# Kernel optimization log

Measured on AMD Instinct MI355X. Metric: run time of the kernel, lower is better.

The kernel has to match this reference:

```python
import jax, jax.numpy as jnp
import numpy as np

HEADS = 8
DIM_HEAD = 64
BOTTLENECK = 40


def setup_inputs() -> dict:
    key = jax.random.key(0)
    ks = jax.random.split(key, 10)
    b, n, qs = 4, 1024, 256
    inner = HEADS * DIM_HEAD
    s = lambda fan_in: 1.0 / np.sqrt(fan_in)
    return {
        "x":   jax.random.normal(ks[0], (b, n, qs), dtype=jnp.float32),
        # weights stored as (in, out) so forward is x @ W
        "wq1": jax.random.normal(ks[1], (qs, BOTTLENECK), dtype=jnp.float32) * s(qs),
        "wq2": jax.random.normal(ks[2], (BOTTLENECK, inner), dtype=jnp.float32) * s(BOTTLENECK),
        "wk1": jax.random.normal(ks[3], (qs, BOTTLENECK), dtype=jnp.float32) * s(qs),
        "wk2": jax.random.normal(ks[4], (BOTTLENECK, inner), dtype=jnp.float32) * s(BOTTLENECK),
        "wv1": jax.random.normal(ks[5], (qs, BOTTLENECK), dtype=jnp.float32) * s(qs),
        "wv2": jax.random.normal(ks[6], (BOTTLENECK, inner), dtype=jnp.float32) * s(BOTTLENECK),
        "wo":  jax.random.normal(ks[7], (inner, qs), dtype=jnp.float32) * s(inner),
        "bo":  jax.random.normal(ks[8], (qs,), dtype=jnp.float32) * 0.01,
    }


def reference(x, wq1, wq2, wk1, wk2, wv1, wv2, wo, bo):
    b, n, _ = x.shape
    h, d = HEADS, DIM_HEAD
    scale = d ** -0.5

    # bottlenecked QKV projections (40-dim), SiLU on K bottleneck
    q = (x @ wq1) @ wq2                       # (b, n, h*d)
    k = jax.nn.silu(x @ wk1) @ wk2            # (b, n, h*d)
    v = (x @ wv1) @ wv2                       # (b, n, h*d)

    def split(t):  # 'b n (h d) -> b (h n) d'
        return t.reshape(b, n, h, d).transpose(0, 2, 1, 3).reshape(b, h * n, d)

    q, k, v = split(q), split(k), split(v)

    sim = jnp.einsum('bid,bjd->bij', q, k) * scale   # (b, h*n, h*n)
    attn = jax.nn.softmax(sim, axis=-1)
    out = jnp.einsum('bij,bjd->bid', attn, v)        # (b, h*n, d)

    # 'b (h n) d -> b n (h d)'
    out = out.reshape(b, h, n, d).transpose(0, 2, 1, 3).reshape(b, n, h * d)
    return out @ wo + bo
```

## Files before the change

kernel.cpp:

```cpp
#include <hip/hip_runtime.h>
#include <hip/hip_bf16.h>


#define B_    4
#define H_    8
#define NSEQ  1024
#define SEQ   8192
#define DH    64
#define QS    256
#define INNER 512
#define QSCALE 0.18033688011112042f

#define KVSW_BATCH 524288

typedef __bf16 bf16x8 __attribute__((ext_vector_type(8)));
typedef float floatx4 __attribute__((ext_vector_type(4)));

__global__ __launch_bounds__(512, 4) void qkv_kernel(
    const float* __restrict__ x,
    const float* __restrict__ wq1, const float* __restrict__ wq2,
    const float* __restrict__ wk1, const float* __restrict__ wk2,
    const float* __restrict__ wv1, const float* __restrict__ wv2,
    __hip_bfloat16* __restrict__ Qg, __hip_bfloat16* __restrict__ KSg,
    __hip_bfloat16* __restrict__ VSg)
{
  const int tid  = threadIdx.x;
  const int p    = blockIdx.x >> 8;
  const int rest = blockIdx.x & 255;
  const int b    = rest >> 6;
  const int nblk = rest & 63;
  const int n0   = nblk << 4;

  __shared__ __align__(16) float xs[16][260];
  __shared__ __align__(16) float tb2[4][16][40];
  __shared__ __align__(16) float tb[16][40];
  __shared__ __align__(16) __hip_bfloat16 ob[10400];

  const float* w1 = (p == 0) ? wq1 : (p == 1) ? wk1 : wv1;
  const float* w2 = (p == 0) ? wq2 : (p == 1) ? wk2 : wv2;

  #pragma unroll
  for (int j = 0; j < 2; ++j) {
    const int i  = tid + j * 512;
    const int r  = i >> 6;
    const int c4 = (i & 63) << 2;
    *(float4*)(&xs[r][c4]) =
        *(const float4*)(x + ((size_t)b * NSEQ + n0 + r) * QS + c4);
  }
  __syncthreads();

  for (int t = tid; t < 640; t += 512) {
    const int ks  = t / 160;
    const int rem = t - ks * 160;
    const int r   = rem / 10;
    const int bn  = (rem - r * 10) * 4;
    float a0 = 0.f, a1 = 0.f, a2 = 0.f, a3 = 0.f;
    #pragma unroll 4
    for (int c4 = ks * 16; c4 < ks * 16 + 16; ++c4) {
      const float4 xv = *(const float4*)(&xs[r][c4 * 4]);
      const float4 wa = *(const float4*)(w1 + (c4 * 4 + 0) * 40 + bn);
      const float4 wb = *(const float4*)(w1 + (c4 * 4 + 1) * 40 + bn);
      const float4 wc = *(const float4*)(w1 + (c4 * 4 + 2) * 40 + bn);
      const float4 wd = *(const float4*)(w1 + (c4 * 4 + 3) * 40 + bn);
      a0 += xv.x * wa.x + xv.y * wb.x + xv.z * wc.x + xv.w * wd.x;
      a1 += xv.x * wa.y + xv.y * wb.y + xv.z * wc.y + xv.w * wd.y;
      a2 += xv.x * wa.z + xv.y * wb.z + xv.z * wc.z + xv.w * wd.z;
      a3 += xv.x * wa.w + xv.y * wb.w + xv.z * wc.w + xv.w * wd.w;
    }
    tb2[ks][r][bn + 0] = a0; tb2[ks][r][bn + 1] = a1;
    tb2[ks][r][bn + 2] = a2; tb2[ks][r][bn + 3] = a3;
  }
  __syncthreads();

  if (tid < 160) {
    const int r  = tid / 10;
    const int bn = (tid - r * 10) * 4;
    const float4 h0 = *(const float4*)(&tb2[0][r][bn]);
    const float4 h1 = *(const float4*)(&tb2[1][r][bn]);
    const float4 h2 = *(const float4*)(&tb2[2][r][bn]);
    const float4 h3 = *(const float4*)(&tb2[3][r][bn]);
    float a0 = (h0.x + h1.x) + (h2.x + h3.x);
    float a1 = (h0.y + h1.y) + (h2.y + h3.y);
    float a2 = (h0.z + h1.z) + (h2.z + h3.z);
    float a3 = (h0.w + h1.w) + (h2.w + h3.w);
    if (p == 1) {
      a0 = a0 / (1.f + __expf(-a0));
      a1 = a1 / (1.f + __expf(-a1));
      a2 = a2 / (1.f + __expf(-a2));
      a3 = a3 / (1.f + __expf(-a3));
    }
    tb[r][bn + 0] = a0; tb[r][bn + 1] = a1;
    tb[r][bn + 2] = a2; tb[r][bn + 3] = a3;
  }
  __syncthreads();

  {
    const int cq = tid & 127;
    const int rq = tid >> 7;
    const int c  = cq * 4, r0 = rq * 4;
    const float scale = (p == 0) ? QSCALE : 1.0f;
    float acc[4][4];
    #pragma unroll
    for (int i = 0; i < 4; ++i)
      #pragma unroll
      for (int j = 0; j < 4; ++j) acc[i][j] = 0.f;

    #pragma unroll 2
    for (int jb = 0; jb < 10; ++jb) {
      const float4 w0  = *(const float4*)(w2 + (jb * 4 + 0) * INNER + c);
      const float4 w1r = *(const float4*)(w2 + (jb * 4 + 1) * INNER + c);
      const float4 w2r = *(const float4*)(w2 + (jb * 4 + 2) * INNER + c);
      const float4 w3  = *(const float4*)(w2 + (jb * 4 + 3) * INNER + c);
      #pragma unroll
      for (int ri = 0; ri < 4; ++ri) {
        const float4 tv = *(const float4*)(&tb[r0 + ri][jb * 4]);
        acc[ri][0] += tv.x * w0.x + tv.y * w1r.x + tv.z * w2r.x + tv.w * w3.x;
        acc[ri][1] += tv.x * w0.y + tv.y * w1r.y + tv.z * w2r.y + tv.w * w3.y;
        acc[ri][2] += tv.x * w0.z + tv.y * w1r.z + tv.z * w2r.z + tv.w * w3.z;
        acc[ri][3] += tv.x * w0.w + tv.y * w1r.w + tv.z * w2r.w + tv.w * w3.w;
      }
    }
    #pragma unroll
    for (int ri = 0; ri < 4; ++ri)
      #pragma unroll
      for (int ci = 0; ci < 4; ++ci) {
        const int cc = c + ci;
        const float v = acc[ri][ci] * scale;
        if (p == 2) ob[cc * 20 + r0 + ri]    = __float2bfloat16(v);
        else        ob[(r0 + ri) * 520 + cc] = __float2bfloat16(v);
      }
  }
  __syncthreads();

  if (p == 0) {
    #pragma unroll
    for (int j = 0; j < 2; ++j) {
      const int i  = tid + j * 512;
      const int h  = i >> 7;
      const int r  = (i >> 3) & 15;
      const int d8 = i & 7;
      *(float4*)(Qg + ((size_t)b * SEQ + h * NSEQ + n0 + r) * DH + d8 * 8) =
          *(const float4*)(&ob[r * 520 + h * 64 + d8 * 8]);
    }
  } else if (p == 1) {
    #pragma unroll
    for (int j = 0; j < 2; ++j) {
      const int i    = tid + j * 512;
      const int h    = i >> 7;
      const int ks2  = (i >> 6) & 1;
      const int quad = (i >> 4) & 3;
      const int r    = i & 15;
      const int lane = quad * 16 + r;
      const size_t dst = (size_t)b * KVSW_BATCH
          + ((size_t)((h * 64 + nblk) * 2 + ks2) * 64 + lane) * 8;
      *(float4*)(KSg + dst) = *(const float4*)(&ob[r * 520 + h * 64 + ks2 * 32 + quad * 8]);
    }
  } else {
    const int st  = nblk & 1;
    const int p32 = nblk >> 1;
    #pragma unroll
    for (int pass = 0; pass < 4; ++pass) {
      const int i   = tid + pass * 512;
      const int h   = i >> 8;
      const int dnt = (i >> 6) & 3;
      const int dm  = (i >> 2) & 15;
      const int rg  = i & 3;
      const int lane = rg * 16 + dm;
      const size_t dst = (size_t)b * KVSW_BATCH
          + ((size_t)((h * 32 + p32) * 4 + dnt) * 64 + lane) * 8 + st * 4;
      *(uint2*)(VSg + dst) = *(const uint2*)(&ob[(h * 64 + dnt * 16 + dm) * 20 + rg * 4]);
    }
  }
}

struct PairBuf {
  bf16x8 k[2][2];
  bf16x8 v[4];
};

__global__ __launch_bounds__(256, 3) void attn_kernel(
    const __hip_bfloat16* __restrict__ Qg,
    const __hip_bfloat16* __restrict__ KSg,
    const __hip_bfloat16* __restrict__ VSg,
    float* __restrict__ OPg,
    float* __restrict__ PSg)
{
  __shared__ float Osh[4][16][68];
  __shared__ float psums[4][64];

  const int tid  = threadIdx.x;
  const int wave = tid >> 6;
  const int lane = tid & 63;
  const int lrow = lane & 15;
  const int quad = lane >> 4;

  const int xcd   = blockIdx.x & 7;
  const int idx   = blockIdx.x >> 3;
  const int b     = xcd >> 1;
  const int half  = idx & 1;
  const int qtile = (xcd & 1) * 64 + (idx >> 1);
  const int qbase = qtile * 64;

  const __hip_bfloat16* Qb  = Qg + ((size_t)b * SEQ + qbase) * DH;
  const __hip_bfloat16* kp0 = KSg + (size_t)b * KVSW_BATCH + half * 262144
                              + (size_t)wave * 65536 + lane * 8;
  const __hip_bfloat16* vp0 = VSg + (size_t)b * KVSW_BATCH + half * 262144
                              + (size_t)wave * 65536 + lane * 8;

  bf16x8 qf[4][2];
  #pragma unroll
  for (int mt = 0; mt < 4; ++mt)
    #pragma unroll
    for (int s = 0; s < 2; ++s)
      qf[mt][s] = *(const bf16x8*)(Qb + (mt * 16 + lrow) * DH + s * 32 + quad * 8);

  floatx4 oacc[4][4];
  #pragma unroll
  for (int mt = 0; mt < 4; ++mt)
    #pragma unroll
    for (int dnt = 0; dnt < 4; ++dnt)
      oacc[mt][dnt] = (floatx4){0.f, 0.f, 0.f, 0.f};
  float psum[4] = {0.f, 0.f, 0.f, 0.f};

  #pragma unroll 2
  for (int pair = 0; pair < 32; ++pair) {
    PairBuf pb;
    const __hip_bfloat16* kp = kp0 + pair * 2048;
    pb.k[0][0] = *(const bf16x8*)(kp);
    pb.k[0][1] = *(const bf16x8*)(kp + 512);
    pb.k[1][0] = *(const bf16x8*)(kp + 1024);
    pb.k[1][1] = *(const bf16x8*)(kp + 1536);
    const __hip_bfloat16* vp = vp0 + pair * 2048;
    #pragma unroll
    for (int dnt = 0; dnt < 4; ++dnt)
      pb.v[dnt] = *(const bf16x8*)(vp + dnt * 512);

    #pragma unroll
    for (int mt = 0; mt < 4; ++mt) {
      floatx4 s0 = (floatx4){0.f, 0.f, 0.f, 0.f};
      floatx4 s1 = (floatx4){0.f, 0.f, 0.f, 0.f};
      s0 = __builtin_amdgcn_mfma_f32_16x16x32_bf16(pb.k[0][0], qf[mt][0], s0, 0, 0, 0);
      s0 = __builtin_amdgcn_mfma_f32_16x16x32_bf16(pb.k[0][1], qf[mt][1], s0, 0, 0, 0);
      s1 = __builtin_amdgcn_mfma_f32_16x16x32_bf16(pb.k[1][0], qf[mt][0], s1, 0, 0, 0);
      s1 = __builtin_amdgcn_mfma_f32_16x16x32_bf16(pb.k[1][1], qf[mt][1], s1, 0, 0, 0);
      float p[8];
      #pragma unroll
      for (int r = 0; r < 4; ++r) {
        p[r]     = __builtin_amdgcn_exp2f(s0[r]);
        p[4 + r] = __builtin_amdgcn_exp2f(s1[r]);
      }
      psum[mt] += ((p[0] + p[1]) + (p[2] + p[3])) + ((p[4] + p[5]) + (p[6] + p[7]));
      bf16x8 pa;
      #pragma unroll
      for (int j = 0; j < 8; ++j) pa[j] = (__bf16)p[j];
      #pragma unroll
      for (int dnt = 0; dnt < 4; ++dnt)
        oacc[mt][dnt] = __builtin_amdgcn_mfma_f32_16x16x32_bf16(pa, pb.v[dnt], oacc[mt][dnt], 0, 0, 0);
    }
  }

  #pragma unroll
  for (int mt = 0; mt < 4; ++mt) {
    float s = psum[mt];
    s += __shfl_xor(s, 16, 64);
    s += __shfl_xor(s, 32, 64);
    psum[mt] = s;
  }
  if (quad == 0) {
    #pragma unroll
    for (int mt = 0; mt < 4; ++mt)
      psums[wave][mt * 16 + lrow] = psum[mt];
  }

  const size_t opbase = ((size_t)half * B_ + b) * SEQ + qbase;

  #pragma unroll
  for (int mt = 0; mt < 4; ++mt) {
    #pragma unroll
    for (int dnt = 0; dnt < 4; ++dnt)
      #pragma unroll
      for (int r = 0; r < 4; ++r)
        Osh[wave][quad * 4 + r][dnt * 16 + lrow] = oacc[mt][dnt][r];
    __syncthreads();

    {
      const int q16 = tid >> 4;
      const int d0  = (tid & 15) * 4;
      float4 a0 = *(const float4*)(&Osh[0][q16][d0]);
      float4 a1 = *(const float4*)(&Osh[1][q16][d0]);
      float4 a2 = *(const float4*)(&Osh[2][q16][d0]);
      float4 a3 = *(const float4*)(&Osh[3][q16][d0]);
      float4 res;
      res.x = (a0.x + a1.x) + (a2.x + a3.x);
      res.y = (a0.y + a1.y) + (a2.y + a3.y);
      res.z = (a0.z + a1.z) + (a2.z + a3.z);
      res.w = (a0.w + a1.w) + (a2.w + a3.w);
      *(float4*)(OPg + (opbase + mt * 16 + q16) * DH + d0) = res;
    }
    if (mt == 0 && tid < 64) {
      const float tot = (psums[0][tid] + psums[1][tid]) + (psums[2][tid] + psums[3][tid]);
      PSg[opbase + tid] = tot;
    }
    __syncthreads();
  }
}

__global__ __launch_bounds__(512) void out_kernel(
    const float* __restrict__ OPg, const float* __restrict__ PSg,
    const float* __restrict__ wo, const float* __restrict__ bo,
    float* __restrict__ out)
{
  const int tid = threadIdx.x;
  const int b   = blockIdx.x >> 6;
  const int n0  = (blockIdx.x & 63) << 4;

  __shared__ __align__(16) float os[16][520];
  __shared__ __align__(16) float wot[2][16][260];
  __shared__ float invs[16][8];

  if (tid < 128) {
    const int r = tid >> 3, h = tid & 7;
    const size_t row = (size_t)b * SEQ + h * NSEQ + n0 + r;
    invs[r][h] = 1.0f / (PSg[row] + PSg[(size_t)B_ * SEQ + row]);
  }
  __syncthreads();

  for (int i = tid; i < 2048; i += 512) {
    const int r  = i >> 7;
    const int c4 = (i & 127) * 4;
    const int h  = c4 >> 6;
    const size_t idx = ((size_t)b * SEQ + h * NSEQ + n0 + r) * DH + (c4 & 63);
    const float4 p0 = *(const float4*)(OPg + idx);
    const float4 p1 = *(const float4*)(OPg + (size_t)B_ * SEQ * DH + idx);
    const float inv = invs[r][c4 >> 6];
    float4 m;
    m.x = (p0.x + p1.x) * inv;
    m.y = (p0.y + p1.y) * inv;
    m.z = (p0.z + p1.z) * inv;
    m.w = (p0.w + p1.w) * inv;
    *(float4*)(&os[r][c4]) = m;
  }

  {
    const int c0 = tid, c1 = tid + 512;
    const float4 v0 = *(const float4*)(wo + (size_t)(c0 >> 6) * QS + (c0 & 63) * 4);
    const float4 v1 = *(const float4*)(wo + (size_t)(c1 >> 6) * QS + (c1 & 63) * 4);
    *(float4*)(&wot[0][c0 >> 6][(c0 & 63) * 4]) = v0;
    *(float4*)(&wot[0][c1 >> 6][(c1 & 63) * 4]) = v1;
  }
  __syncthreads();

  const int oq = tid & 63;
  const int rq = tid >> 6;
  const int o  = oq * 4;
  const int r0 = rq * 2;

  float acc[2][4];
  #pragma unroll
  for (int i = 0; i < 2; ++i)
    #pragma unroll
    for (int j = 0; j < 4; ++j) acc[i][j] = 0.f;

  for (int kt = 0; kt < 32; ++kt) {
    const int cur = kt & 1;
    float4 pf0, pf1;
    const int c0 = tid, c1 = tid + 512;
    if (kt < 31) {
      const int kb = (kt + 1) * 16;
      pf0 = *(const float4*)(wo + (size_t)(kb + (c0 >> 6)) * QS + (c0 & 63) * 4);
      pf1 = *(const float4*)(wo + (size_t)(kb + (c1 >> 6)) * QS + (c1 & 63) * 4);
    }

    const int kbase = kt * 16;
    #pragma unroll
    for (int kq = 0; kq < 4; ++kq) {
      const float4 ov0 = *(const float4*)(&os[r0][kbase + kq * 4]);
      const float4 ov1 = *(const float4*)(&os[r0 + 1][kbase + kq * 4]);
      #pragma unroll
      for (int j = 0; j < 4; ++j) {
        const float4 w = *(const float4*)(&wot[cur][kq * 4 + j][o]);
        const float a = (j == 0) ? ov0.x : (j == 1) ? ov0.y : (j == 2) ? ov0.z : ov0.w;
        const float bq = (j == 0) ? ov1.x : (j == 1) ? ov1.y : (j == 2) ? ov1.z : ov1.w;
        acc[0][0] += a * w.x; acc[0][1] += a * w.y;
        acc[0][2] += a * w.z; acc[0][3] += a * w.w;
        acc[1][0] += bq * w.x; acc[1][1] += bq * w.y;
        acc[1][2] += bq * w.z; acc[1][3] += bq * w.w;
      }
    }

    if (kt < 31) {
      *(float4*)(&wot[cur ^ 1][c0 >> 6][(c0 & 63) * 4]) = pf0;
      *(float4*)(&wot[cur ^ 1][c1 >> 6][(c1 & 63) * 4]) = pf1;
    }
    __syncthreads();
  }

  const float4 bv = *(const float4*)(bo + o);
  #pragma unroll
  for (int ri = 0; ri < 2; ++ri) {
    float4 res;
    res.x = acc[ri][0] + bv.x;
    res.y = acc[ri][1] + bv.y;
    res.z = acc[ri][2] + bv.z;
    res.w = acc[ri][3] + bv.w;
    *(float4*)(out + ((size_t)b * NSEQ + n0 + r0 + ri) * QS + o) = res;
  }
}

extern "C" void kernel_launch(void* const* d_in, const int* in_sizes, int n_in,
                              void* d_out, int out_size, void* d_ws, size_t ws_size,
                              hipStream_t stream) {
  const float* x   = (const float*)d_in[0];
  const float* wq1 = (const float*)d_in[1];
  const float* wq2 = (const float*)d_in[2];
  const float* wk1 = (const float*)d_in[3];
  const float* wk2 = (const float*)d_in[4];
  const float* wv1 = (const float*)d_in[5];
  const float* wv2 = (const float*)d_in[6];
  const float* wo  = (const float*)d_in[7];
  const float* bo  = (const float*)d_in[8];
  float* out = (float*)d_out;

  __hip_bfloat16* Qg  = (__hip_bfloat16*)d_ws;
  __hip_bfloat16* KSg = Qg + (size_t)B_ * SEQ * DH;
  __hip_bfloat16* VSg = KSg + (size_t)B_ * KVSW_BATCH;
  float*          OPg = (float*)(VSg + (size_t)B_ * KVSW_BATCH);
  float*          PSg = OPg + 2 * (size_t)B_ * SEQ * DH;

  qkv_kernel<<<768, 512, 0, stream>>>(x, wq1, wq2, wk1, wk2, wv1, wv2, Qg, KSg, VSg);
  attn_kernel<<<1024, 256, 0, stream>>>(Qg, KSg, VSg, OPg, PSg);
  out_kernel<<<256, 512, 0, stream>>>(OPg, PSg, wo, bo, out);
}
```

Baseline: 191.9 us.

## Move output projection to bf16 split-precision MFMA with pre-swizzled wo

Rewrites the output projection to use bf16 MFMA with a hi/lo split (three products) instead of scalar fp32 FMA. Extra blocks in the QKV kernel convert wo into hi/lo bf16 fragments in MFMA-ready layout each call, and the attention partial outputs are normalized, split, and staged in LDS. This targets the FP32 ALU cost of the final GEMM and adds conversion work plus some precision loss from dropping the lo*lo term.

```diff
diff --git a/kernel.cpp b/kernel.cpp
--- a/kernel.cpp
+++ b/kernel.cpp
@@ -12,6 +12,7 @@
 #define QSCALE 0.18033688011112042f
 
 #define KVSW_BATCH 524288
+#define OPHALF (2097152)
 
 typedef __bf16 bf16x8 __attribute__((ext_vector_type(8)));
 typedef float floatx4 __attribute__((ext_vector_type(4)));
@@ -21,10 +22,43 @@
     const float* __restrict__ wq1, const float* __restrict__ wq2,
     const float* __restrict__ wk1, const float* __restrict__ wk2,
     const float* __restrict__ wv1, const float* __restrict__ wv2,
+    const float* __restrict__ wo,
     __hip_bfloat16* __restrict__ Qg, __hip_bfloat16* __restrict__ KSg,
-    __hip_bfloat16* __restrict__ VSg)
+    __hip_bfloat16* __restrict__ VSg,
+    __hip_bfloat16* __restrict__ WOBH, __hip_bfloat16* __restrict__ WOBL)
 {
   const int tid  = threadIdx.x;
+
+  if (blockIdx.x >= 768) {
+    const int cid = blockIdx.x - 768;
+    const int t4  = (cid * 512 + tid) * 4;
+    const int n   = t4 & 255;
+    const int k8  = t4 >> 8;
+    float4 rr[8];
+    #pragma unroll
+    for (int kk = 0; kk < 8; ++kk)
+      rr[kk] = *(const float4*)(wo + (size_t)(k8 * 8 + kk) * QS + n);
+    const int kc = k8 >> 2, qq = k8 & 3;
+    #pragma unroll
+    for (int nn = 0; nn < 4; ++nn) {
+      const int nc = n + nn;
+      const int l  = (nc & 15) + 16 * qq;
+      const size_t off = ((size_t)((nc >> 4) * 16 + kc) * 64 + l) * 8;
+      bf16x8 hv, lv;
+      #pragma unroll
+      for (int kk = 0; kk < 8; ++kk) {
+        const float v = (nn == 0) ? rr[kk].x : (nn == 1) ? rr[kk].y
+                      : (nn == 2) ? rr[kk].z : rr[kk].w;
+        const __bf16 h16 = (__bf16)v;
+        hv[kk] = h16;
+        lv[kk] = (__bf16)(v - (float)h16);
+      }
+      *(bf16x8*)(WOBH + off) = hv;
+      *(bf16x8*)(WOBL + off) = lv;
+    }
+    return;
+  }
+
   const int p    = blockIdx.x >> 8;
   const int rest = blockIdx.x & 255;
   const int b    = rest >> 6;
@@ -305,18 +339,20 @@
   }
 }
 
-__global__ __launch_bounds__(512) void out_kernel(
+__global__ __launch_bounds__(256, 1) void out_kernel(
     const float* __restrict__ OPg, const float* __restrict__ PSg,
-    const float* __restrict__ wo, const float* __restrict__ bo,
-    float* __restrict__ out)
+    const __hip_bfloat16* __restrict__ WOBH, const __hip_bfloat16* __restrict__ WOBL,
+    const float* __restrict__ bo, float* __restrict__ out)
 {
-  const int tid = threadIdx.x;
-  const int b   = blockIdx.x >> 6;
-  const int n0  = (blockIdx.x & 63) << 4;
-
-  __shared__ __align__(16) float os[16][520];
-  __shared__ __align__(16) float wot[2][16][260];
+  __shared__ __align__(16) __hip_bfloat16 apH[8192];
+  __shared__ __align__(16) __hip_bfloat16 apL[8192];
   __shared__ float invs[16][8];
+
+  const int tid  = threadIdx.x;
+  const int b    = blockIdx.x >> 6;
+  const int n0   = (blockIdx.x & 63) << 4;
+  const int lane = tid & 63;
+  const int wave = tid >> 6;
 
   if (tid < 128) {
     const int r = tid >> 3, h = tid & 7;
@@ -325,85 +361,82 @@
   }
   __syncthreads();
 
-  for (int i = tid; i < 2048; i += 512) {
-    const int r  = i >> 7;
-    const int c4 = (i & 127) * 4;
-    const int h  = c4 >> 6;
-    const size_t idx = ((size_t)b * SEQ + h * NSEQ + n0 + r) * DH + (c4 & 63);
-    const float4 p0 = *(const float4*)(OPg + idx);
-    const float4 p1 = *(const float4*)(OPg + (size_t)B_ * SEQ * DH + idx);
-    const float inv = invs[r][c4 >> 6];
-    float4 m;
-    m.x = (p0.x + p1.x) * inv;
-    m.y = (p0.y + p1.y) * inv;
-    m.z = (p0.z + p1.z) * inv;
-    m.w = (p0.w + p1.w) * inv;
-    *(float4*)(&os[r][c4]) = m;
-  }
-
   {
-    const int c0 = tid, c1 = tid + 512;
-    const float4 v0 = *(const float4*)(wo + (size_t)(c0 >> 6) * QS + (c0 & 63) * 4);
-    const float4 v1 = *(const float4*)(wo + (size_t)(c1 >> 6) * QS + (c1 & 63) * 4);
-    *(float4*)(&wot[0][c0 >> 6][(c0 & 63) * 4]) = v0;
-    *(float4*)(&wot[0][c1 >> 6][(c1 & 63) * 4]) = v1;
-  }
-  __syncthreads();
-
-  const int oq = tid & 63;
-  const int rq = tid >> 6;
-  const int o  = oq * 4;
-  const int r0 = rq * 2;
-
-  float acc[2][4];
-  #pragma unroll
-  for (int i = 0; i < 2; ++i)
-    #pragma unroll
-    for (int j = 0; j < 4; ++j) acc[i][j] = 0.f;
-
-  for (int kt = 0; kt < 32; ++kt) {
-    const int cur = kt & 1;
-    float4 pf0, pf1;
-    const int c0 = tid, c1 = tid + 512;
-    if (kt < 31) {
-      const int kb = (kt + 1) * 16;
-      pf0 = *(const float4*)(wo + (size_t)(kb + (c0 >> 6)) * QS + (c0 & 63) * 4);
-      pf1 = *(const float4*)(wo + (size_t)(kb + (c1 >> 6)) * QS + (c1 & 63) * 4);
-    }
-
-    const int kbase = kt * 16;
-    #pragma unroll
-    for (int kq = 0; kq < 4; ++kq) {
-      const float4 ov0 = *(const float4*)(&os[r0][kbase + kq * 4]);
-      const float4 ov1 = *(const float4*)(&os[r0 + 1][kbase + kq * 4]);
+    const int m   = tid & 15;
+    const int q   = (tid >> 4) & 3;
+    const int kc0 = tid >> 6;
+    #pragma unroll
+    for (int pss = 0; pss < 4; ++pss) {
+      const int kc = kc0 + pss * 4;
+      const int h  = kc >> 1;
+      const int dh = (q + 4 * (kc & 1)) * 8;
+      const size_t idx = (((size_t)b * H_ + h) * NSEQ + n0 + m) * DH + dh;
+      const float4 a0 = *(const float4*)(OPg + idx);
+      const float4 a1 = *(const float4*)(OPg + idx + 4);
+      const float4 b0 = *(const float4*)(OPg + OPHALF + idx);
+      const float4 b1 = *(const float4*)(OPg + OPHALF + idx + 4);
+      const float inv = invs[m][h];
+      float v[8];
+      v[0] = (a0.x + b0.x) * inv; v[1] = (a0.y + b0.y) * inv;
+      v[2] = (a0.z + b0.z) * inv; v[3] = (a0.w + b0.w) * inv;
+      v[4] = (a1.x + b1.x) * inv; v[5] = (a1.y + b1.y) * inv;
+      v[6] = (a1.z + b1.z) * inv; v[7] = (a1.w + b1.w) * inv;
+      bf16x8 hv, lv;
+      #pragma unroll
+      for (int j = 0; j < 8; ++j) {
+        const __bf16 h16 = (__bf16)v[j];
+        hv[j] = h16;
+        lv[j] = (__bf16)(v[j] - (float)h16);
+      }
+      const int off = (kc * 64 + (m + 16 * q)) * 8;
+      *(bf16x8*)(apH + off) = hv;
+      *(bf16x8*)(apL + off) = lv;
+    }
+  }
+  __syncthreads();
+
+  bf16x8 ah[16], al[16];
+  #pragma unroll
+  for (int kc = 0; kc < 16; ++kc) {
+    ah[kc] = *(const bf16x8*)(apH + (kc * 64 + lane) * 8);
+    al[kc] = *(const bf16x8*)(apL + (kc * 64 + lane) * 8);
+  }
+
+  const int colq = lane & 15;
+  const int quad = lane >> 4;
+
+  #pragma unroll
+  for (int nt4 = 0; nt4 < 4; ++nt4) {
+    const int nt = nt4 * 4 + wave;
+    const __hip_bfloat16* wbh = WOBH + ((size_t)nt * 16 * 64 + lane) * 8;
+    const __hip_bfloat16* wbl = WOBL + ((size_t)nt * 16 * 64 + lane) * 8;
+    floatx4 aHH = (floatx4){0.f, 0.f, 0.f, 0.f};
+    floatx4 aHL = (floatx4){0.f, 0.f, 0.f, 0.f};
+    floatx4 aLH = (floatx4){0.f, 0.f, 0.f, 0.f};
+    #pragma unroll
+    for (int kg = 0; kg < 4; ++kg) {
+      bf16x8 bh[4], bl[4];
       #pragma unroll
       for (int j = 0; j < 4; ++j) {
-        const float4 w = *(const float4*)(&wot[cur][kq * 4 + j][o]);
-        const float a = (j == 0) ? ov0.x : (j == 1) ? ov0.y : (j == 2) ? ov0.z : ov0.w;
-        const float bq = (j == 0) ? ov1.x : (j == 1) ? ov1.y : (j == 2) ? ov1.z : ov1.w;
-        acc[0][0] += a * w.x; acc[0][1] += a * w.y;
-        acc[0][2] += a * w.z; acc[0][3] += a * w.w;
-        acc[1][0] += bq * w.x; acc[1][1] += bq * w.y;
-        acc[1][2] += bq * w.z; acc[1][3] += bq * w.w;
-      }
-    }
-
-    if (kt < 31) {
-      *(float4*)(&wot[cur ^ 1][c0 >> 6][(c0 & 63) * 4]) = pf0;
-      *(float4*)(&wot[cur ^ 1][c1 >> 6][(c1 & 63) * 4]) = pf1;
-    }
-    __syncthreads();
-  }
-
-  const float4 bv = *(const float4*)(bo + o);
-  #pragma unroll
-  for (int ri = 0; ri < 2; ++ri) {
-    float4 res;
-    res.x = acc[ri][0] + bv.x;
-    res.y = acc[ri][1] + bv.y;
-    res.z = acc[ri][2] + bv.z;
-    res.w = acc[ri][3] + bv.w;
-    *(float4*)(out + ((size_t)b * NSEQ + n0 + r0 + ri) * QS + o) = res;
+        bh[j] = *(const bf16x8*)(wbh + (kg * 4 + j) * 512);
+        bl[j] = *(const bf16x8*)(wbl + (kg * 4 + j) * 512);
+      }
+      #pragma unroll
+      for (int j = 0; j < 4; ++j) {
+        const int kc = kg * 4 + j;
+        aHH = __builtin_amdgcn_mfma_f32_16x16x32_bf16(ah[kc], bh[j], aHH, 0, 0, 0);
+        aHL = __builtin_amdgcn_mfma_f32_16x16x32_bf16(ah[kc], bl[j], aHL, 0, 0, 0);
+        aLH = __builtin_amdgcn_mfma_f32_16x16x32_bf16(al[kc], bh[j], aLH, 0, 0, 0);
+      }
+    }
+    const int n  = nt * 16 + colq;
+    const float bv = bo[n];
+    #pragma unroll
+    for (int r = 0; r < 4; ++r) {
+      const int mm = quad * 4 + r;
+      out[((size_t)b * NSEQ + n0 + mm) * QS + n] =
+          ((aHH[r] + aHL[r]) + aLH[r]) + bv;
+    }
   }
 }
 
@@ -426,8 +459,11 @@
   __hip_bfloat16* VSg = KSg + (size_t)B_ * KVSW_BATCH;
   float*          OPg = (float*)(VSg + (size_t)B_ * KVSW_BATCH);
   float*          PSg = OPg + 2 * (size_t)B_ * SEQ * DH;
-
-  qkv_kernel<<<768, 512, 0, stream>>>(x, wq1, wq2, wk1, wk2, wv1, wv2, Qg, KSg, VSg);
+  __hip_bfloat16* WOBH = (__hip_bfloat16*)(PSg + 2 * (size_t)B_ * SEQ);
+  __hip_bfloat16* WOBL = WOBH + (size_t)INNER * QS;
+
+  qkv_kernel<<<776, 512, 0, stream>>>(x, wq1, wq2, wk1, wk2, wv1, wv2, wo,
+                                      Qg, KSg, VSg, WOBH, WOBL);
   attn_kernel<<<1024, 256, 0, stream>>>(Qg, KSg, VSg, OPg, PSg);
-  out_kernel<<<256, 512, 0, stream>>>(OPg, PSg, wo, bo, out);
+  out_kernel<<<256, 256, 0, stream>>>(OPg, PSg, WOBH, WOBL, bo, out);
 }
```

Measured after the change: 179.9 us. -6.2%, faster.
